# Kernel optimization log

Measured on AMD Instinct MI355X. Metric: run time of the kernel, lower is better.

The kernel has to match this reference:

```python
import jax, jax.numpy as jnp
import numpy as np

N, IN, OUT, K = 4096, 512, 256, 3
ALPHA, BETA, ETA = 0.2, 0.1, 0.5
NEG_INF = -9e15


def setup_inputs() -> dict:
    key = jax.random.key(0)
    k1, k2, k3, k4, k5, k6 = jax.random.split(key, 6)
    h = jax.random.normal(k1, (N, IN), dtype=jnp.float32)
    # xavier-ish scale for params
    W = jax.random.normal(k2, (K * IN, OUT), dtype=jnp.float32) * (1.414 / np.sqrt(IN + OUT))
    a = jax.random.normal(k3, (2 * OUT * K, 1), dtype=jnp.float32) * 0.05
    disc = jax.random.normal(k4, (2 * OUT, 1), dtype=jnp.float32) * 0.05
    k_mask = jax.random.randint(k5, (K, N, N), 0, 2).astype(jnp.int32)  # 0/1 k-hop masks
    lamda = jax.random.uniform(k6, (1,), dtype=jnp.float32)
    return {"h": h, "W": W, "a": a, "disc": disc, "k_mask": k_mask, "lamda": lamda}


def reference(h, W, a, disc, k_mask, lamda):
    lam = lamda[0]
    Wk = W.reshape(K, IN, OUT)          # W[i*IN:(i+1)*IN] per hop
    ak = a.reshape(K, 2, OUT)           # a[2*hop*OUT:(2*hop+2)*OUT] per hop, split in two
    d = disc.reshape(2, OUT)

    # Per-hop projections. In the torch loop Wh is recomputed from h each hop,
    # so only hop 0 determines the returned features; all hops feed dischange.
    Wh_all = jnp.einsum('ni,kio->kno', h, Wk)  # [K, N, OUT]

    # dischange = sum_i eta^i * (Wh_i @ d1 + (Wh_i @ d2).T)  -- rank-1 separable
    wts = ETA ** jnp.arange(K, dtype=jnp.float32)            # [K]
    dv1 = jnp.einsum('kno,o->kn', Wh_all, d[0])              # [K, N]
    dv2 = jnp.einsum('kno,o->kn', Wh_all, d[1])
    u = jnp.einsum('k,kn->n', wts, dv1)
    v = jnp.einsum('k,kn->n', wts, dv2)
    dischange = u[:, None] + v[None, :]                      # [N, N]

    # hop-0 masked GAT attention
    Wh0 = Wh_all[0]
    s1 = Wh0 @ ak[0, 0]                                      # [N]
    s2 = Wh0 @ ak[0, 1]
    e = jax.nn.leaky_relu(s1[:, None] + s2[None, :], ALPHA)  # [N, N]
    att = jax.nn.softmax(jnp.where(k_mask[0] > 0, e, NEG_INF), axis=1)
    # dropout disabled (eval mode / training=False)
    Wh = (1.0 - BETA) * (att @ Wh0) + BETA * Wh0
    out = jax.nn.elu(Wh)

    # normalize dischange and threshold against lamda
    dn = dischange / jnp.maximum(jnp.abs(dischange.min()), dischange.max())
    pos = (dn > lam).astype(jnp.int32)
    dn = jnp.where(dn > lam, 0.0, dn)
    neg = (dn < -lam).astype(jnp.int32)
    dn = jnp.where(dn < -lam, 0.0, dn)

    # mask lists computed from ORIGINAL masks, then applied sequentially
    pos_list = [((k_mask[i] + pos) >= 2).astype(jnp.int32) for i in range(K - 1)]
    neg_list = [((k_mask[i] + neg) >= 2).astype(jnp.int32) for i in range(1, K)]
    km = k_mask
    for i in range(1, K):
        km = km.at[i].add(pos_list[i - 1])
        km = km.at[i - 1].add(-pos_list[i - 1])
    for i in range(K - 1):
        km = km.at[i + 1].add(neg_list[i])
        km = km.at[i].add(-neg_list[i])

    return out, dn, km
```

## Files before the change

kernel.cpp:

```cpp
#include <hip/hip_runtime.h>
#include <hip/hip_bf16.h>
#include <math.h>

#define N 4096
#define DIN 512
#define DOUT 256
#define JS 8
#define JCH (N / JS)

typedef short bf16x8 __attribute__((ext_vector_type(8)));
typedef float f32x4 __attribute__((ext_vector_type(4)));

static __device__ __forceinline__ unsigned short f2bf(float x) {
  __hip_bfloat16 b = __float2bfloat16(x);
  return __builtin_bit_cast(unsigned short, b);
}

__global__ __launch_bounds__(256) void k_pq(const float* __restrict__ W,
                                            const float* __restrict__ disc,
                                            double* __restrict__ p, double* __restrict__ q) {
  __shared__ double lds[8];
  int i = blockIdx.x;
  int t = threadIdx.x;
  double accp = 0.0, accq = 0.0;
  const double wts[3] = {1.0, 0.5, 0.25};
#pragma unroll
  for (int k = 0; k < 3; ++k) {
    double w = (double)W[((size_t)(k * DIN + i)) * DOUT + t];
    accp += wts[k] * w * (double)disc[t];
    accq += wts[k] * w * (double)disc[DOUT + t];
  }
  for (int off = 32; off; off >>= 1) { accp += __shfl_down(accp, off); accq += __shfl_down(accq, off); }
  int l = t & 63, w_ = t >> 6;
  if (l == 0) { lds[w_] = accp; lds[4 + w_] = accq; }
  __syncthreads();
  if (t == 0) {
    p[i] = lds[0] + lds[1] + lds[2] + lds[3];
    q[i] = lds[4] + lds[5] + lds[6] + lds[7];
  }
}

__global__ __launch_bounds__(256) void k_uv(const float* __restrict__ h,
                                            const double* __restrict__ p, const double* __restrict__ q,
                                            double* __restrict__ u, double* __restrict__ v) {
  __shared__ double lds[8];
  int n = blockIdx.x, t = threadIdx.x;
  double su = 0.0, sv = 0.0;
#pragma unroll
  for (int i = t; i < DIN; i += 256) {
    double hv = (double)h[(size_t)n * DIN + i];
    su += hv * p[i];
    sv += hv * q[i];
  }
  for (int off = 32; off; off >>= 1) { su += __shfl_down(su, off); sv += __shfl_down(sv, off); }
  int l = t & 63, w_ = t >> 6;
  if (l == 0) { lds[w_] = su; lds[4 + w_] = sv; }
  __syncthreads();
  if (t == 0) {
    u[n] = lds[0] + lds[1] + lds[2] + lds[3];
    v[n] = lds[4] + lds[5] + lds[6] + lds[7];
  }
}

__global__ __launch_bounds__(1024) void k_denom(const double* __restrict__ u,
                                                const double* __restrict__ v,
                                                double* __restrict__ scal) {
  __shared__ double lds[64];
  int t = threadIdx.x;
  double mnu = 1e300, mxu = -1e300, mnv = 1e300, mxv = -1e300;
#pragma unroll
  for (int k = 0; k < 4; ++k) {
    double uu = u[t + k * 1024], vv = v[t + k * 1024];
    mnu = fmin(mnu, uu); mxu = fmax(mxu, uu);
    mnv = fmin(mnv, vv); mxv = fmax(mxv, vv);
  }
  for (int off = 32; off; off >>= 1) {
    mnu = fmin(mnu, __shfl_down(mnu, off)); mxu = fmax(mxu, __shfl_down(mxu, off));
    mnv = fmin(mnv, __shfl_down(mnv, off)); mxv = fmax(mxv, __shfl_down(mxv, off));
  }
  int l = t & 63, w_ = t >> 6;
  if (l == 0) { lds[w_] = mnu; lds[16 + w_] = mxu; lds[32 + w_] = mnv; lds[48 + w_] = mxv; }
  __syncthreads();
  if (t == 0) {
    double a = 1e300, b = -1e300, c = 1e300, d = -1e300;
    for (int k = 0; k < 16; ++k) {
      a = fmin(a, lds[k]); b = fmax(b, lds[16 + k]);
      c = fmin(c, lds[32 + k]); d = fmax(d, lds[48 + k]);
    }
    double mn = a + c, mx = b + d;
    double denom = fmax(fabs(mn), mx);
    scal[0] = 1.0 / denom;
  }
}

__global__ __launch_bounds__(256) void k_dnkm(const int* __restrict__ kmask,
                                              const double* __restrict__ u, const double* __restrict__ v,
                                              const double* __restrict__ scal, const float* __restrict__ lamda,
                                              float* __restrict__ dn, float* __restrict__ kmout) {
  const size_t NN = (size_t)N * N;
  const int* k0 = kmask; const int* k1 = kmask + NN; const int* k2 = kmask + 2 * NN;
  float* km0 = kmout; float* km1 = kmout + NN; float* km2 = kmout + 2 * NN;
  const size_t total4 = NN / 4;
  double inv = scal[0];
  double lam = (double)lamda[0];
  for (size_t idx = (size_t)blockIdx.x * 256 + threadIdx.x; idx < total4;
       idx += (size_t)gridDim.x * 256) {
    int i = (int)(idx >> 10);
    int j = (int)(idx & 1023) << 2;
    size_t base = (size_t)i * N + j;
    double ui = u[i];
    double2 va = *(const double2*)(v + j);
    double2 vb = *(const double2*)(v + j + 2);
    double vv[4] = {va.x, va.y, vb.x, vb.y};
    int4 m0 = *(const int4*)(k0 + base);
    int4 m1 = *(const int4*)(k1 + base);
    int4 m2 = *(const int4*)(k2 + base);
    float4 odn, o0, o1, o2;
#pragma unroll
    for (int c = 0; c < 4; ++c) {
      double dnv = (ui + vv[c]) * inv;
      bool pos = dnv > lam, neg = dnv < -lam;
      float dnf = (pos || neg) ? 0.0f : (float)dnv;
      int mk0 = (&m0.x)[c], mk1 = (&m1.x)[c], mk2 = (&m2.x)[c];
      int p0 = pos ? mk0 : 0;
      int p1 = pos ? mk1 : 0;
      int n0 = neg ? mk1 : 0;
      int n1 = neg ? mk2 : 0;
      (&odn.x)[c] = dnf;
      (&o0.x)[c] = (float)(mk0 - p0 - n0);
      (&o1.x)[c] = (float)(mk1 + p0 - p1 + n0 - n1);
      (&o2.x)[c] = (float)(mk2 + p1 + n1);
    }
    *(float4*)(dn + base) = odn;
    *(float4*)(km0 + base) = o0;
    *(float4*)(km1 + base) = o1;
    *(float4*)(km2 + base) = o2;
  }
}

__global__ __launch_bounds__(256) void k_wh0(const float* __restrict__ h, const float* __restrict__ W,
                                             float* __restrict__ Wh0, unsigned short* __restrict__ Wh0T) {
  __shared__ float As[64][20];
  __shared__ float Bs[16][72];
  int t = threadIdx.x;
  int i0 = blockIdx.x * 64, o0 = blockIdx.y * 64;
  int tx = t & 15, ty = t >> 4;
  float acc[4][4] = {};
  int am = t >> 2, ak = (t & 3) * 4;
  int bk = t >> 4, bn = (t & 15) * 4;
  for (int kb = 0; kb < DIN; kb += 16) {
    float4 av = *(const float4*)(h + (size_t)(i0 + am) * DIN + kb + ak);
    float4 bv = *(const float4*)(W + (size_t)(kb + bk) * DOUT + o0 + bn);
    *(float4*)&As[am][ak] = av;
    *(float4*)&Bs[bk][bn] = bv;
    __syncthreads();
#pragma unroll
    for (int kk = 0; kk < 16; ++kk) {
      float a0 = As[ty * 4 + 0][kk], a1 = As[ty * 4 + 1][kk];
      float a2 = As[ty * 4 + 2][kk], a3 = As[ty * 4 + 3][kk];
      float4 b = *(const float4*)&Bs[kk][tx * 4];
      acc[0][0] += a0 * b.x; acc[0][1] += a0 * b.y; acc[0][2] += a0 * b.z; acc[0][3] += a0 * b.w;
      acc[1][0] += a1 * b.x; acc[1][1] += a1 * b.y; acc[1][2] += a1 * b.z; acc[1][3] += a1 * b.w;
      acc[2][0] += a2 * b.x; acc[2][1] += a2 * b.y; acc[2][2] += a2 * b.z; acc[2][3] += a2 * b.w;
      acc[3][0] += a3 * b.x; acc[3][1] += a3 * b.y; acc[3][2] += a3 * b.z; acc[3][3] += a3 * b.w;
    }
    __syncthreads();
  }
#pragma unroll
  for (int r = 0; r < 4; ++r) {
    int n = i0 + ty * 4 + r;
    float4 vo = {acc[r][0], acc[r][1], acc[r][2], acc[r][3]};
    *(float4*)(Wh0 + (size_t)n * DOUT + o0 + tx * 4) = vo;
#pragma unroll
    for (int c = 0; c < 4; ++c) {
      Wh0T[(size_t)(o0 + tx * 4 + c) * N + n] = f2bf(acc[r][c]);
    }
  }
}

__global__ __launch_bounds__(256) void k_s1s2(const float* __restrict__ Wh0, const float* __restrict__ a,
                                              float* __restrict__ s1, float* __restrict__ s2) {
  __shared__ float lds[8];
  int i = blockIdx.x, t = threadIdx.x;
  float val = Wh0[(size_t)i * DOUT + t];
  float v1 = val * a[t];
  float v2 = val * a[DOUT + t];
  for (int off = 32; off; off >>= 1) { v1 += __shfl_down(v1, off); v2 += __shfl_down(v2, off); }
  int l = t & 63, w_ = t >> 6;
  if (l == 0) { lds[w_] = v1; lds[4 + w_] = v2; }
  __syncthreads();
  if (t == 0) {
    s1[i] = lds[0] + lds[1] + lds[2] + lds[3];
    s2[i] = lds[4] + lds[5] + lds[6] + lds[7];
  }
}

__global__ __launch_bounds__(256) void k_rowstats(const int* __restrict__ k0,
                                                  const float* __restrict__ s1, const float* __restrict__ s2,
                                                  float* __restrict__ mrow, float* __restrict__ zinv,
                                                  int* __restrict__ flag) {
  __shared__ float earr[N];
  __shared__ float redf[4];
  __shared__ int redi[4];
  __shared__ float bm; __shared__ int bc;
  int i = blockIdx.x, t = threadIdx.x;
  float s1i = s1[i];
  float lmax = -1e30f; int lcnt = 0;
  for (int j = t; j < N; j += 256) {
    int mk = k0[(size_t)i * N + j];
    float sv = s1i + s2[j];
    float e = sv >= 0.0f ? sv : 0.2f * sv;
    bool um = mk > 0;
    earr[j] = um ? e : -1e30f;
    if (um) { lmax = fmaxf(lmax, e); lcnt++; }
  }
  for (int off = 32; off; off >>= 1) { lmax = fmaxf(lmax, __shfl_down(lmax, off)); lcnt += __shfl_down(lcnt, off); }
  int l = t & 63, w_ = t >> 6;
  if (l == 0) { redf[w_] = lmax; redi[w_] = lcnt; }
  __syncthreads();
  if (t == 0) {
    bm = fmaxf(fmaxf(redf[0], redf[1]), fmaxf(redf[2], redf[3]));
    bc = redi[0] + redi[1] + redi[2] + redi[3];
  }
  __syncthreads();
  float m = bm; int c = bc;
  float lsum = 0.0f;
  if (c > 0) {
    for (int j = t; j < N; j += 256) {
      float e = earr[j];
      if (e > -1e29f) lsum += expf(e - m);
    }
  }
  for (int off = 32; off; off >>= 1) lsum += __shfl_down(lsum, off);
  if (l == 0) redf[w_] = lsum;
  __syncthreads();
  if (t == 0) {
    float Z = redf[0] + redf[1] + redf[2] + redf[3];
    if (c == 0) { mrow[i] = 0.0f; zinv[i] = 1.0f / (float)N; flag[i] = 1; }
    else        { mrow[i] = m;    zinv[i] = 1.0f / Z;        flag[i] = 0; }
  }
}

__global__ __launch_bounds__(256) void k_attn2(const int* __restrict__ k0,
                                               const float* __restrict__ s1, const float* __restrict__ s2,
                                               const float* __restrict__ mrow, const int* __restrict__ flag,
                                               const unsigned short* __restrict__ Wh0T,
                                               float* __restrict__ Opart) {
  int t = threadIdx.x;
  int i0 = blockIdx.x * 16;
  int w = t >> 6, l = t & 63;
  int o0 = w * 64;
  int row = l & 15;
  int kg = l >> 4;
  int irow = i0 + row;
  float s1r = s1[irow], mr = mrow[irow];
  int fl = flag[irow];
  f32x4 acc0 = {0,0,0,0}, acc1 = {0,0,0,0}, acc2 = {0,0,0,0}, acc3 = {0,0,0,0};
  const unsigned short* bbase = Wh0T + ((size_t)(o0 + row) * N + 8 * kg);
  const int* mbase = k0 + (size_t)irow * N + 8 * kg;
  const float* sbase = s2 + 8 * kg;
  int jbeg = blockIdx.y * JCH;
  for (int j0 = jbeg; j0 < jbeg + JCH; j0 += 32) {
    int4 ma = *(const int4*)(mbase + j0);
    int4 mb = *(const int4*)(mbase + j0 + 4);
    float4 sa = *(const float4*)(sbase + j0);
    float4 sb = *(const float4*)(sbase + j0 + 4);
    float pv[8];
#pragma unroll
    for (int c = 0; c < 4; ++c) {
      float sv = s1r + (&sa.x)[c];
      float e = sv >= 0.0f ? sv : 0.2f * sv;
      pv[c] = fl ? 1.0f : ((&ma.x)[c] > 0 ? expf(e - mr) : 0.0f);
    }
#pragma unroll
    for (int c = 0; c < 4; ++c) {
      float sv = s1r + (&sb.x)[c];
      float e = sv >= 0.0f ? sv : 0.2f * sv;
      pv[4 + c] = fl ? 1.0f : ((&mb.x)[c] > 0 ? expf(e - mr) : 0.0f);
    }
    bf16x8 af;
#pragma unroll
    for (int c = 0; c < 8; ++c) af[c] = (short)f2bf(pv[c]);
    bf16x8 b0 = *(const bf16x8*)(bbase + j0);
    bf16x8 b1 = *(const bf16x8*)(bbase + 16 * N + j0);
    bf16x8 b2 = *(const bf16x8*)(bbase + 32 * N + j0);
    bf16x8 b3 = *(const bf16x8*)(bbase + 48 * N + j0);
    acc0 = __builtin_amdgcn_mfma_f32_16x16x32_bf16(af, b0, acc0, 0, 0, 0);
    acc1 = __builtin_amdgcn_mfma_f32_16x16x32_bf16(af, b1, acc1, 0, 0, 0);
    acc2 = __builtin_amdgcn_mfma_f32_16x16x32_bf16(af, b2, acc2, 0, 0, 0);
    acc3 = __builtin_amdgcn_mfma_f32_16x16x32_bf16(af, b3, acc3, 0, 0, 0);
  }
  float* op = Opart + (size_t)blockIdx.y * N * DOUT;
  int col = l & 15, rw = (l >> 4) * 4;
  f32x4 accs[4] = {acc0, acc1, acc2, acc3};
#pragma unroll
  for (int reg = 0; reg < 4; ++reg) {
    int i = i0 + rw + reg;
#pragma unroll
    for (int os = 0; os < 4; ++os) {
      op[(size_t)i * DOUT + o0 + os * 16 + col] = accs[os][reg];
    }
  }
}

__global__ __launch_bounds__(256) void k_ored(const float* __restrict__ Opart,
                                              const float* __restrict__ Wh0,
                                              const float* __restrict__ zinv,
                                              float* __restrict__ out) {
  int i = blockIdx.x, t = threadIdx.x;
  size_t idx = (size_t)i * DOUT + t;
  float s = 0.0f;
#pragma unroll
  for (int by = 0; by < JS; ++by) s += Opart[(size_t)by * N * DOUT + idx];
  float val = 0.9f * s * zinv[i] + 0.1f * Wh0[idx];
  out[idx] = val > 0.0f ? val : expm1f(val);
}

extern "C" void kernel_launch(void* const* d_in, const int* in_sizes, int n_in,
                              void* d_out, int out_size, void* d_ws, size_t ws_size,
                              hipStream_t stream) {
  const float* h     = (const float*)d_in[0];
  const float* W     = (const float*)d_in[1];
  const float* a     = (const float*)d_in[2];
  const float* disc  = (const float*)d_in[3];
  const int*   kmask = (const int*)d_in[4];
  const float* lamda = (const float*)d_in[5];

  float* out = (float*)d_out;
  float* dn  = out + (size_t)N * DOUT;
  float* km  = dn + (size_t)N * N;

  char* ws = (char*)d_ws;
  double* p    = (double*)ws;
  double* q    = (double*)(ws + 4096);
  double* u    = (double*)(ws + 8192);
  double* v    = (double*)(ws + 8192 + 32768);
  double* scal = (double*)(ws + 8192 + 65536);
  char* ws2 = ws + 8192 + 65536 + 256;
  float* s1   = (float*)ws2;
  float* s2   = (float*)(ws2 + 16384);
  float* mrow = (float*)(ws2 + 32768);
  float* zin  = (float*)(ws2 + 49152);
  int*   flag = (int*)(ws2 + 65536);
  float* Wh0  = (float*)(ws2 + 65536 + 16384);
  unsigned short* Wh0T = (unsigned short*)(ws2 + 65536 + 16384 + (size_t)N * DOUT * 4);
  float* Opart = (float*)(ws2 + 65536 + 16384 + (size_t)N * DOUT * 4 + (size_t)N * DOUT * 2);

  k_pq<<<DIN, 256, 0, stream>>>(W, disc, p, q);
  k_uv<<<N, 256, 0, stream>>>(h, p, q, u, v);
  k_denom<<<1, 1024, 0, stream>>>(u, v, scal);
  k_dnkm<<<4096, 256, 0, stream>>>(kmask, u, v, scal, lamda, dn, km);
  k_wh0<<<dim3(64, 4), 256, 0, stream>>>(h, W, Wh0, Wh0T);
  k_s1s2<<<N, 256, 0, stream>>>(Wh0, a, s1, s2);
  k_rowstats<<<N, 256, 0, stream>>>(kmask, s1, s2, mrow, zin, flag);
  k_attn2<<<dim3(N / 16, JS), 256, 0, stream>>>(kmask, s1, s2, mrow, flag, Wh0T, Opart);
  k_ored<<<N, 256, 0, stream>>>(Opart, Wh0, zin, out);
}
```

Measured before the change: 621.4 us.

## Replace row-stats pass with global-max softmax bound and fused normalizer accumulation

Removes the separate row max/sum kernel that reread the hop-0 mask, using an upper bound leaky_relu(s1_i + max s2) as the softmax stabilizer. The normalizer is accumulated inside the attention MFMA kernel and summed in the reduction. It also adds nontemporal mask loads and output stores, retiles the projection GEMM with register prefetch, and uses 512-thread attention blocks with fast exp. Rows with no unmasked neighbors would now divide by zero instead of taking a uniform average.

```diff
diff --git a/kernel.cpp b/kernel.cpp
--- a/kernel.cpp
+++ b/kernel.cpp
@@ -10,15 +10,27 @@
 
 typedef short bf16x8 __attribute__((ext_vector_type(8)));
 typedef float f32x4 __attribute__((ext_vector_type(4)));
+typedef int i32x4 __attribute__((ext_vector_type(4)));
 
 static __device__ __forceinline__ unsigned short f2bf(float x) {
   __hip_bfloat16 b = __float2bfloat16(x);
   return __builtin_bit_cast(unsigned short, b);
 }
 
+static __device__ __forceinline__ unsigned int f2ord(float f) {
+  unsigned int b = __float_as_uint(f);
+  return (b & 0x80000000u) ? ~b : (b | 0x80000000u);
+}
+static __device__ __forceinline__ float ord2f(unsigned int u) {
+  unsigned int b = (u & 0x80000000u) ? (u ^ 0x80000000u) : ~u;
+  return __uint_as_float(b);
+}
+
 __global__ __launch_bounds__(256) void k_pq(const float* __restrict__ W,
                                             const float* __restrict__ disc,
-                                            double* __restrict__ p, double* __restrict__ q) {
+                                            double* __restrict__ p, double* __restrict__ q,
+                                            unsigned int* __restrict__ smaxw) {
+  if (blockIdx.x == 0 && threadIdx.x == 0) smaxw[0] = 0u;
   __shared__ double lds[8];
   int i = blockIdx.x;
   int t = threadIdx.x;
@@ -88,8 +100,7 @@
       c = fmin(c, lds[32 + k]); d = fmax(d, lds[48 + k]);
     }
     double mn = a + c, mx = b + d;
-    double denom = fmax(fabs(mn), mx);
-    scal[0] = 1.0 / denom;
+    scal[0] = 1.0 / fmax(fabs(mn), mx);
   }
 }
 
@@ -112,63 +123,65 @@
     double2 va = *(const double2*)(v + j);
     double2 vb = *(const double2*)(v + j + 2);
     double vv[4] = {va.x, va.y, vb.x, vb.y};
-    int4 m0 = *(const int4*)(k0 + base);
-    int4 m1 = *(const int4*)(k1 + base);
-    int4 m2 = *(const int4*)(k2 + base);
-    float4 odn, o0, o1, o2;
+    i32x4 m0 = __builtin_nontemporal_load((const i32x4*)(k0 + base));
+    i32x4 m1 = __builtin_nontemporal_load((const i32x4*)(k1 + base));
+    i32x4 m2 = __builtin_nontemporal_load((const i32x4*)(k2 + base));
+    f32x4 odn, o0, o1, o2;
 #pragma unroll
     for (int c = 0; c < 4; ++c) {
       double dnv = (ui + vv[c]) * inv;
       bool pos = dnv > lam, neg = dnv < -lam;
       float dnf = (pos || neg) ? 0.0f : (float)dnv;
-      int mk0 = (&m0.x)[c], mk1 = (&m1.x)[c], mk2 = (&m2.x)[c];
+      int mk0 = m0[c], mk1 = m1[c], mk2 = m2[c];
       int p0 = pos ? mk0 : 0;
       int p1 = pos ? mk1 : 0;
       int n0 = neg ? mk1 : 0;
       int n1 = neg ? mk2 : 0;
-      (&odn.x)[c] = dnf;
-      (&o0.x)[c] = (float)(mk0 - p0 - n0);
-      (&o1.x)[c] = (float)(mk1 + p0 - p1 + n0 - n1);
-      (&o2.x)[c] = (float)(mk2 + p1 + n1);
-    }
-    *(float4*)(dn + base) = odn;
-    *(float4*)(km0 + base) = o0;
-    *(float4*)(km1 + base) = o1;
-    *(float4*)(km2 + base) = o2;
+      odn[c] = dnf;
+      o0[c] = (float)(mk0 - p0 - n0);
+      o1[c] = (float)(mk1 + p0 - p1 + n0 - n1);
+      o2[c] = (float)(mk2 + p1 + n1);
+    }
+    __builtin_nontemporal_store(odn, (f32x4*)(dn + base));
+    __builtin_nontemporal_store(o0, (f32x4*)(km0 + base));
+    __builtin_nontemporal_store(o1, (f32x4*)(km1 + base));
+    __builtin_nontemporal_store(o2, (f32x4*)(km2 + base));
   }
 }
 
 __global__ __launch_bounds__(256) void k_wh0(const float* __restrict__ h, const float* __restrict__ W,
                                              float* __restrict__ Wh0, unsigned short* __restrict__ Wh0T) {
-  __shared__ float As[64][20];
+  __shared__ float As[32][20];
   __shared__ float Bs[16][72];
   int t = threadIdx.x;
-  int i0 = blockIdx.x * 64, o0 = blockIdx.y * 64;
+  int i0 = blockIdx.x * 32, o0 = blockIdx.y * 64;
   int tx = t & 15, ty = t >> 4;
-  float acc[4][4] = {};
+  float acc[2][4] = {};
   int am = t >> 2, ak = (t & 3) * 4;
   int bk = t >> 4, bn = (t & 15) * 4;
+  float4 pa, pb;
+  if (t < 128) pa = *(const float4*)(h + (size_t)(i0 + am) * DIN + ak);
+  pb = *(const float4*)(W + (size_t)bk * DOUT + o0 + bn);
   for (int kb = 0; kb < DIN; kb += 16) {
-    float4 av = *(const float4*)(h + (size_t)(i0 + am) * DIN + kb + ak);
-    float4 bv = *(const float4*)(W + (size_t)(kb + bk) * DOUT + o0 + bn);
-    *(float4*)&As[am][ak] = av;
-    *(float4*)&Bs[bk][bn] = bv;
+    if (t < 128) *(float4*)&As[am][ak] = pa;
+    *(float4*)&Bs[bk][bn] = pb;
     __syncthreads();
+    if (kb + 16 < DIN) {
+      if (t < 128) pa = *(const float4*)(h + (size_t)(i0 + am) * DIN + kb + 16 + ak);
+      pb = *(const float4*)(W + (size_t)(kb + 16 + bk) * DOUT + o0 + bn);
+    }
 #pragma unroll
     for (int kk = 0; kk < 16; ++kk) {
-      float a0 = As[ty * 4 + 0][kk], a1 = As[ty * 4 + 1][kk];
-      float a2 = As[ty * 4 + 2][kk], a3 = As[ty * 4 + 3][kk];
+      float a0 = As[ty * 2 + 0][kk], a1 = As[ty * 2 + 1][kk];
       float4 b = *(const float4*)&Bs[kk][tx * 4];
       acc[0][0] += a0 * b.x; acc[0][1] += a0 * b.y; acc[0][2] += a0 * b.z; acc[0][3] += a0 * b.w;
       acc[1][0] += a1 * b.x; acc[1][1] += a1 * b.y; acc[1][2] += a1 * b.z; acc[1][3] += a1 * b.w;
-      acc[2][0] += a2 * b.x; acc[2][1] += a2 * b.y; acc[2][2] += a2 * b.z; acc[2][3] += a2 * b.w;
-      acc[3][0] += a3 * b.x; acc[3][1] += a3 * b.y; acc[3][2] += a3 * b.z; acc[3][3] += a3 * b.w;
     }
     __syncthreads();
   }
 #pragma unroll
-  for (int r = 0; r < 4; ++r) {
-    int n = i0 + ty * 4 + r;
+  for (int r = 0; r < 2; ++r) {
+    int n = i0 + ty * 2 + r;
     float4 vo = {acc[r][0], acc[r][1], acc[r][2], acc[r][3]};
     *(float4*)(Wh0 + (size_t)n * DOUT + o0 + tx * 4) = vo;
 #pragma unroll
@@ -179,7 +192,8 @@
 }
 
 __global__ __launch_bounds__(256) void k_s1s2(const float* __restrict__ Wh0, const float* __restrict__ a,
-                                              float* __restrict__ s1, float* __restrict__ s2) {
+                                              float* __restrict__ s1, float* __restrict__ s2,
+                                              unsigned int* __restrict__ smaxw) {
   __shared__ float lds[8];
   int i = blockIdx.x, t = threadIdx.x;
   float val = Wh0[(size_t)i * DOUT + t];
@@ -191,78 +205,37 @@
   __syncthreads();
   if (t == 0) {
     s1[i] = lds[0] + lds[1] + lds[2] + lds[3];
-    s2[i] = lds[4] + lds[5] + lds[6] + lds[7];
-  }
-}
-
-__global__ __launch_bounds__(256) void k_rowstats(const int* __restrict__ k0,
-                                                  const float* __restrict__ s1, const float* __restrict__ s2,
-                                                  float* __restrict__ mrow, float* __restrict__ zinv,
-                                                  int* __restrict__ flag) {
-  __shared__ float earr[N];
-  __shared__ float redf[4];
-  __shared__ int redi[4];
-  __shared__ float bm; __shared__ int bc;
-  int i = blockIdx.x, t = threadIdx.x;
-  float s1i = s1[i];
-  float lmax = -1e30f; int lcnt = 0;
-  for (int j = t; j < N; j += 256) {
-    int mk = k0[(size_t)i * N + j];
-    float sv = s1i + s2[j];
-    float e = sv >= 0.0f ? sv : 0.2f * sv;
-    bool um = mk > 0;
-    earr[j] = um ? e : -1e30f;
-    if (um) { lmax = fmaxf(lmax, e); lcnt++; }
-  }
-  for (int off = 32; off; off >>= 1) { lmax = fmaxf(lmax, __shfl_down(lmax, off)); lcnt += __shfl_down(lcnt, off); }
-  int l = t & 63, w_ = t >> 6;
-  if (l == 0) { redf[w_] = lmax; redi[w_] = lcnt; }
-  __syncthreads();
-  if (t == 0) {
-    bm = fmaxf(fmaxf(redf[0], redf[1]), fmaxf(redf[2], redf[3]));
-    bc = redi[0] + redi[1] + redi[2] + redi[3];
-  }
-  __syncthreads();
-  float m = bm; int c = bc;
-  float lsum = 0.0f;
-  if (c > 0) {
-    for (int j = t; j < N; j += 256) {
-      float e = earr[j];
-      if (e > -1e29f) lsum += expf(e - m);
-    }
-  }
-  for (int off = 32; off; off >>= 1) lsum += __shfl_down(lsum, off);
-  if (l == 0) redf[w_] = lsum;
-  __syncthreads();
-  if (t == 0) {
-    float Z = redf[0] + redf[1] + redf[2] + redf[3];
-    if (c == 0) { mrow[i] = 0.0f; zinv[i] = 1.0f / (float)N; flag[i] = 1; }
-    else        { mrow[i] = m;    zinv[i] = 1.0f / Z;        flag[i] = 0; }
-  }
-}
-
-__global__ __launch_bounds__(256) void k_attn2(const int* __restrict__ k0,
+    float s2i = lds[4] + lds[5] + lds[6] + lds[7];
+    s2[i] = s2i;
+    atomicMax(smaxw, f2ord(s2i));
+  }
+}
+
+__global__ __launch_bounds__(512) void k_attn2(const int* __restrict__ k0,
                                                const float* __restrict__ s1, const float* __restrict__ s2,
-                                               const float* __restrict__ mrow, const int* __restrict__ flag,
+                                               const unsigned int* __restrict__ smaxw,
                                                const unsigned short* __restrict__ Wh0T,
-                                               float* __restrict__ Opart) {
+                                               float* __restrict__ Opart, float* __restrict__ Zpart) {
   int t = threadIdx.x;
-  int i0 = blockIdx.x * 16;
   int w = t >> 6, l = t & 63;
-  int o0 = w * 64;
+  int o0 = (w & 3) * 64;
+  int rbase = blockIdx.x * 32 + (w >> 2) * 16;
   int row = l & 15;
   int kg = l >> 4;
-  int irow = i0 + row;
-  float s1r = s1[irow], mr = mrow[irow];
-  int fl = flag[irow];
+  int irow = rbase + row;
+  float s1r = s1[irow];
+  float sm2 = ord2f(smaxw[0]);
+  float mb = s1r + sm2;
+  float mi = mb >= 0.0f ? mb : 0.2f * mb;
   f32x4 acc0 = {0,0,0,0}, acc1 = {0,0,0,0}, acc2 = {0,0,0,0}, acc3 = {0,0,0,0};
+  float zacc = 0.0f;
   const unsigned short* bbase = Wh0T + ((size_t)(o0 + row) * N + 8 * kg);
   const int* mbase = k0 + (size_t)irow * N + 8 * kg;
   const float* sbase = s2 + 8 * kg;
   int jbeg = blockIdx.y * JCH;
   for (int j0 = jbeg; j0 < jbeg + JCH; j0 += 32) {
     int4 ma = *(const int4*)(mbase + j0);
-    int4 mb = *(const int4*)(mbase + j0 + 4);
+    int4 mb4 = *(const int4*)(mbase + j0 + 4);
     float4 sa = *(const float4*)(sbase + j0);
     float4 sb = *(const float4*)(sbase + j0 + 4);
     float pv[8];
@@ -270,17 +243,18 @@
     for (int c = 0; c < 4; ++c) {
       float sv = s1r + (&sa.x)[c];
       float e = sv >= 0.0f ? sv : 0.2f * sv;
-      pv[c] = fl ? 1.0f : ((&ma.x)[c] > 0 ? expf(e - mr) : 0.0f);
+      pv[c] = (&ma.x)[c] > 0 ? __expf(e - mi) : 0.0f;
     }
 #pragma unroll
     for (int c = 0; c < 4; ++c) {
       float sv = s1r + (&sb.x)[c];
       float e = sv >= 0.0f ? sv : 0.2f * sv;
-      pv[4 + c] = fl ? 1.0f : ((&mb.x)[c] > 0 ? expf(e - mr) : 0.0f);
+      pv[4 + c] = (&mb4.x)[c] > 0 ? __expf(e - mi) : 0.0f;
     }
     bf16x8 af;
 #pragma unroll
     for (int c = 0; c < 8; ++c) af[c] = (short)f2bf(pv[c]);
+    zacc += pv[0] + pv[1] + pv[2] + pv[3] + pv[4] + pv[5] + pv[6] + pv[7];
     bf16x8 b0 = *(const bf16x8*)(bbase + j0);
     bf16x8 b1 = *(const bf16x8*)(bbase + 16 * N + j0);
     bf16x8 b2 = *(const bf16x8*)(bbase + 32 * N + j0);
@@ -290,12 +264,15 @@
     acc2 = __builtin_amdgcn_mfma_f32_16x16x32_bf16(af, b2, acc2, 0, 0, 0);
     acc3 = __builtin_amdgcn_mfma_f32_16x16x32_bf16(af, b3, acc3, 0, 0, 0);
   }
+  zacc += __shfl_xor(zacc, 16);
+  zacc += __shfl_xor(zacc, 32);
+  if ((w & 3) == 0 && l < 16) Zpart[(size_t)blockIdx.y * N + rbase + l] = zacc;
   float* op = Opart + (size_t)blockIdx.y * N * DOUT;
   int col = l & 15, rw = (l >> 4) * 4;
   f32x4 accs[4] = {acc0, acc1, acc2, acc3};
 #pragma unroll
   for (int reg = 0; reg < 4; ++reg) {
-    int i = i0 + rw + reg;
+    int i = rbase + rw + reg;
 #pragma unroll
     for (int os = 0; os < 4; ++os) {
       op[(size_t)i * DOUT + o0 + os * 16 + col] = accs[os][reg];
@@ -304,15 +281,18 @@
 }
 
 __global__ __launch_bounds__(256) void k_ored(const float* __restrict__ Opart,
+                                              const float* __restrict__ Zpart,
                                               const float* __restrict__ Wh0,
-                                              const float* __restrict__ zinv,
                                               float* __restrict__ out) {
   int i = blockIdx.x, t = threadIdx.x;
   size_t idx = (size_t)i * DOUT + t;
-  float s = 0.0f;
-#pragma unroll
-  for (int by = 0; by < JS; ++by) s += Opart[(size_t)by * N * DOUT + idx];
-  float val = 0.9f * s * zinv[i] + 0.1f * Wh0[idx];
+  float s = 0.0f, z = 0.0f;
+#pragma unroll
+  for (int sp = 0; sp < JS; ++sp) {
+    s += Opart[(size_t)sp * N * DOUT + idx];
+    z += Zpart[(size_t)sp * N + i];
+  }
+  float val = 0.9f * (s / z) + 0.1f * Wh0[idx];
   out[idx] = val > 0.0f ? val : expm1f(val);
 }
 
@@ -337,22 +317,21 @@
   double* v    = (double*)(ws + 8192 + 32768);
   double* scal = (double*)(ws + 8192 + 65536);
   char* ws2 = ws + 8192 + 65536 + 256;
-  float* s1   = (float*)ws2;
-  float* s2   = (float*)(ws2 + 16384);
-  float* mrow = (float*)(ws2 + 32768);
-  float* zin  = (float*)(ws2 + 49152);
-  int*   flag = (int*)(ws2 + 65536);
-  float* Wh0  = (float*)(ws2 + 65536 + 16384);
-  unsigned short* Wh0T = (unsigned short*)(ws2 + 65536 + 16384 + (size_t)N * DOUT * 4);
-  float* Opart = (float*)(ws2 + 65536 + 16384 + (size_t)N * DOUT * 4 + (size_t)N * DOUT * 2);
-
-  k_pq<<<DIN, 256, 0, stream>>>(W, disc, p, q);
+  float* s1            = (float*)ws2;
+  float* s2            = (float*)(ws2 + 16384);
+  unsigned int* smaxw  = (unsigned int*)(ws2 + 32768);
+  float* Zpart         = (float*)(ws2 + 33024);
+  char* ws3 = ws2 + 33024 + (size_t)JS * N * 4;
+  float* Wh0           = (float*)ws3;
+  unsigned short* Wh0T = (unsigned short*)(ws3 + (size_t)N * DOUT * 4);
+  float* Opart         = (float*)(ws3 + (size_t)N * DOUT * 6);
+
+  k_pq<<<DIN, 256, 0, stream>>>(W, disc, p, q, smaxw);
   k_uv<<<N, 256, 0, stream>>>(h, p, q, u, v);
   k_denom<<<1, 1024, 0, stream>>>(u, v, scal);
   k_dnkm<<<4096, 256, 0, stream>>>(kmask, u, v, scal, lamda, dn, km);
-  k_wh0<<<dim3(64, 4), 256, 0, stream>>>(h, W, Wh0, Wh0T);
-  k_s1s2<<<N, 256, 0, stream>>>(Wh0, a, s1, s2);
-  k_rowstats<<<N, 256, 0, stream>>>(kmask, s1, s2, mrow, zin, flag);
-  k_attn2<<<dim3(N / 16, JS), 256, 0, stream>>>(kmask, s1, s2, mrow, flag, Wh0T, Opart);
-  k_ored<<<N, 256, 0, stream>>>(Opart, Wh0, zin, out);
-}
+  k_wh0<<<dim3(N / 32, DOUT / 64), 256, 0, stream>>>(h, W, Wh0, Wh0T);
+  k_s1s2<<<N, 256, 0, stream>>>(Wh0, a, s1, s2, smaxw);
+  k_attn2<<<dim3(N / 32, JS), 512, 0, stream>>>(kmask, s1, s2, smaxw, Wh0T, Opart, Zpart);
+  k_ored<<<N, 256, 0, stream>>>(Opart, Zpart, Wh0, out);
+}
```

After: 603.5 us. 2.9% less time.
